# Optimization experiments

Hardware: AMD Instinct MI355X
Metric: run time of the kernel (lower is better)

Reference implementation:

```python
import jax, jax.numpy as jnp
import numpy as np

B, L, D, MAXL = 4, 2048, 1024, 4096

def setup_inputs() -> dict:
    key = jax.random.key(0)
    ks = jax.random.split(key, 7)
    x = jax.random.normal(ks[0], (B, L, D), dtype=jnp.float32)
    mask = jnp.ones((B, 1, L), dtype=jnp.int32)
    # kv_proj: Linear(D,D) -> ReLU -> Linear(D, 2D)
    s1 = 1.0 / np.sqrt(D)
    W1 = jax.random.uniform(ks[1], (D, D), minval=-s1, maxval=s1, dtype=jnp.float32)
    b1 = jax.random.uniform(ks[2], (D,), minval=-s1, maxval=s1, dtype=jnp.float32)
    W2 = jax.random.uniform(ks[3], (D, 2 * D), minval=-s1, maxval=s1, dtype=jnp.float32)
    b2 = jax.random.uniform(ks[4], (2 * D,), minval=-s1, maxval=s1, dtype=jnp.float32)
    D_to_L = jax.random.normal(ks[5], (D, MAXL), dtype=jnp.float32) * 0.01
    return {"x": x, "mask": mask, "W1": W1, "b1": b1, "W2": W2, "b2": b2, "D_to_L": D_to_L}

def reference(x, mask, W1, b1, W2, b2, D_to_L):
    Lcur = x.shape[1]
    h = jax.nn.relu(x @ W1 + b1)          # [B,L,D]
    kv = h @ W2 + b2                       # [B,L,2D]
    k, value = jnp.split(kv, 2, axis=-1)   # [B,L,D] each
    scores = jnp.einsum('bld,dk->blk', k, D_to_L[:, :Lcur])  # [B,L,L]
    scores = jnp.where(mask == 0, -jnp.inf, scores)
    attention = jax.nn.softmax(scores, axis=-1)
    output = attention @ value             # [B,L,D]
    return output, attention
```

## Files before the change

### kernel.cpp

```cpp
#include <hip/hip_runtime.h>
#include <cstdint>
#include <cstddef>

__device__ __forceinline__ float bf2f(uint16_t u) {
    union { uint32_t i; float f; } w; w.i = ((uint32_t)u) << 16; return w.f;
}
__device__ __forceinline__ uint16_t f2bf(float f) {
    union { float f; uint32_t i; } w; w.f = f;
    uint32_t x = w.i;
    uint32_t r = (x + 0x7FFFu + ((x >> 16) & 1u)) >> 16;
    return (uint16_t)r;
}

typedef __bf16 bf16x8 __attribute__((ext_vector_type(8)));
typedef float  f32x4  __attribute__((ext_vector_type(4)));

__device__ __forceinline__ void load_lds16(const void* gptr, void* lptr) {
    __builtin_amdgcn_global_load_lds(
        (__attribute__((address_space(1))) void*)gptr,
        (__attribute__((address_space(3))) void*)lptr,
        16, 0, 0);
}

template<int AFP32, int OUTFP32, int RELU>
__global__ __launch_bounds__(256, 3)
void gemm_bt(const void* __restrict__ Av, const uint16_t* __restrict__ BT,
             const float* __restrict__ bias, void* __restrict__ Cv,
             int K, int lda, int ldb, int ldc,
             long long sA, long long sB, long long sC)
{
    __shared__ uint16_t As[128 * 32];
    __shared__ uint16_t Bs[128 * 32];

    const int nx = (int)gridDim.x, ny = (int)gridDim.y, nz = (int)gridDim.z;
    const int g   = (int)blockIdx.x + nx * ((int)blockIdx.y + ny * (int)blockIdx.z);
    const int xcd = g & 7;
    const int ii  = g >> 3;
    const int xz  = 8 / nz;
    const int bz  = xcd / xz;
    const int sub = xcd % xz;
    const int ypc = ny / xz;
    const int by  = sub * ypc + ii % ypc;
    const int bx  = ii / ypc;

    const int t    = threadIdx.x;
    const int lane = t & 63;
    const int w    = t >> 6;
    const int quad = lane >> 4;
    const int l15  = lane & 15;
    const int wr   = w >> 1;
    const int wc   = w & 1;
    const int gm0  = by * 128;
    const int gn0  = bx * 128;

    BT += (long long)bz * sB;

    f32x4 acc[4][4] = {};

    const int ch_r = lane >> 2;
    const int ch_c = (lane & 3) * 8;

    for (int k0 = 0; k0 < K; k0 += 32) {
        __syncthreads();

        {
            int row = w * 16 + ch_r;
            load_lds16(BT + (size_t)(gn0 + row) * ldb + k0 + ch_c, (void*)(Bs + w * 512));
            load_lds16(BT + (size_t)(gn0 + row + 64) * ldb + k0 + ch_c, (void*)(Bs + (w + 4) * 512));
        }
        if (AFP32) {
            const float* A = (const float*)Av + (long long)bz * sA;
            const int row = t >> 1, half = t & 1;
            const float* ap = A + (size_t)(gm0 + row) * lda + k0 + half * 16;
            float4 f0 = ((const float4*)ap)[0];
            float4 f1 = ((const float4*)ap)[1];
            float4 f2 = ((const float4*)ap)[2];
            float4 f3 = ((const float4*)ap)[3];
            union { __bf16 h[16]; uint4 q[2]; } u;
            u.h[0]  = (__bf16)f0.x; u.h[1]  = (__bf16)f0.y;
            u.h[2]  = (__bf16)f0.z; u.h[3]  = (__bf16)f0.w;
            u.h[4]  = (__bf16)f1.x; u.h[5]  = (__bf16)f1.y;
            u.h[6]  = (__bf16)f1.z; u.h[7]  = (__bf16)f1.w;
            u.h[8]  = (__bf16)f2.x; u.h[9]  = (__bf16)f2.y;
            u.h[10] = (__bf16)f2.z; u.h[11] = (__bf16)f2.w;
            u.h[12] = (__bf16)f3.x; u.h[13] = (__bf16)f3.y;
            u.h[14] = (__bf16)f3.z; u.h[15] = (__bf16)f3.w;
            uint4* d = (uint4*)(As + row * 32 + half * 16);
            d[0] = u.q[0];
            d[1] = u.q[1];
        } else {
            const uint16_t* A = (const uint16_t*)Av + (long long)bz * sA;
            int row = w * 16 + ch_r;
            load_lds16(A + (size_t)(gm0 + row) * lda + k0 + ch_c, (void*)(As + w * 512));
            load_lds16(A + (size_t)(gm0 + row + 64) * lda + k0 + ch_c, (void*)(As + (w + 4) * 512));
        }
        __syncthreads();

        bf16x8 af[4], bfr[4];
#pragma unroll
        for (int i = 0; i < 4; i++) {
            af[i]  = *(const bf16x8*)(As + (wr * 64 + i * 16 + l15) * 32 + quad * 8);
            bfr[i] = *(const bf16x8*)(Bs + (wc * 64 + i * 16 + l15) * 32 + quad * 8);
        }
#pragma unroll
        for (int mi = 0; mi < 4; mi++)
#pragma unroll
            for (int ni = 0; ni < 4; ni++)
                acc[mi][ni] = __builtin_amdgcn_mfma_f32_16x16x32_bf16(af[mi], bfr[ni], acc[mi][ni], 0, 0, 0);
    }

#pragma unroll
    for (int ni = 0; ni < 4; ni++) {
        const int gcol = gn0 + wc * 64 + ni * 16 + l15;
        const float bv = bias ? bias[gcol] : 0.0f;
#pragma unroll
        for (int mi = 0; mi < 4; mi++) {
#pragma unroll
            for (int r = 0; r < 4; r++) {
                const int grow = gm0 + wr * 64 + mi * 16 + quad * 4 + r;
                float v = acc[mi][ni][r] + bv;
                if (RELU) v = fmaxf(v, 0.0f);
                if (OUTFP32) {
                    float* C = (float*)Cv + (long long)bz * sC;
                    C[(size_t)grow * ldc + gcol] = v;
                } else {
                    uint16_t* C = (uint16_t*)Cv + (long long)bz * sC;
                    C[(size_t)grow * ldc + gcol] = f2bf(v);
                }
            }
        }
    }
}

__global__ __launch_bounds__(256)
void transpose_f32_to_bf16(const float* __restrict__ src, uint16_t* __restrict__ dst,
                           int src_ld, int dst_ld)
{
    __shared__ uint16_t tile[64 * 65];
    const int k0 = blockIdx.y * 64, n0 = blockIdx.x * 64;
    const int t = threadIdx.x;
#pragma unroll
    for (int i = 0; i < 16; i++) {
        int idx = i * 256 + t;
        int r = idx >> 6, c = idx & 63;
        tile[c * 65 + r] = f2bf(src[(size_t)(k0 + r) * src_ld + n0 + c]);
    }
    __syncthreads();
#pragma unroll
    for (int i = 0; i < 16; i++) {
        int idx = i * 256 + t;
        int n = idx >> 6, k = idx & 63;
        dst[(size_t)(n0 + n) * dst_ld + k0 + k] = tile[n * 65 + k];
    }
}

__global__ __launch_bounds__(256)
void transpose_bf16(const uint16_t* __restrict__ src, uint16_t* __restrict__ dst,
                    int src_ld, int dst_ld, long long sS, long long sD)
{
    __shared__ uint16_t tile[64 * 65];
    src += (long long)blockIdx.z * sS;
    dst += (long long)blockIdx.z * sD;
    const int k0 = blockIdx.y * 64, n0 = blockIdx.x * 64;
    const int t = threadIdx.x;
#pragma unroll
    for (int i = 0; i < 16; i++) {
        int idx = i * 256 + t;
        int r = idx >> 6, c = idx & 63;
        tile[c * 65 + r] = src[(size_t)(k0 + r) * src_ld + n0 + c];
    }
    __syncthreads();
#pragma unroll
    for (int i = 0; i < 16; i++) {
        int idx = i * 256 + t;
        int n = idx >> 6, k = idx & 63;
        dst[(size_t)(n0 + n) * dst_ld + k0 + k] = tile[n * 65 + k];
    }
}

__global__ __launch_bounds__(256)
void softmax_rows_f32(float* __restrict__ S, uint16_t* __restrict__ Sbf,
                      const int* __restrict__ mask, int L)
{
    const int row = blockIdx.x;
    const int b = row >> 11;
    float* rp = S + (size_t)row * L;
    uint16_t* bp = Sbf + (size_t)row * L;
    const int* mrow = mask + (size_t)b * L;
    const int t = threadIdx.x;
    const int c0 = t * 8;

    float v[8];
    *(float4*)(v + 0) = *(const float4*)(rp + c0);
    *(float4*)(v + 4) = *(const float4*)(rp + c0 + 4);
    bool mk[8];
    float lmax = -1e30f;
#pragma unroll
    for (int j = 0; j < 8; j++) {
        mk[j] = (mrow[c0 + j] != 0);
        if (mk[j]) lmax = fmaxf(lmax, v[j]);
    }
#pragma unroll
    for (int off = 32; off > 0; off >>= 1)
        lmax = fmaxf(lmax, __shfl_xor(lmax, off, 64));

    __shared__ float redm[4];
    __shared__ float reds[4];
    const int w = t >> 6, lane = t & 63;
    if (lane == 0) redm[w] = lmax;
    __syncthreads();
    lmax = fmaxf(fmaxf(redm[0], redm[1]), fmaxf(redm[2], redm[3]));

    float e[8];
    float lsum = 0.f;
#pragma unroll
    for (int j = 0; j < 8; j++) {
        e[j] = mk[j] ? __expf(v[j] - lmax) : 0.0f;
        lsum += e[j];
    }
#pragma unroll
    for (int off = 32; off > 0; off >>= 1)
        lsum += __shfl_xor(lsum, off, 64);
    if (lane == 0) reds[w] = lsum;
    __syncthreads();
    lsum = reds[0] + reds[1] + reds[2] + reds[3];

    const float inv = 1.0f / lsum;
    uint16_t ub[8];
#pragma unroll
    for (int j = 0; j < 8; j++) {
        v[j] = e[j] * inv;
        ub[j] = f2bf(v[j]);
    }
    *(float4*)(rp + c0)     = *(const float4*)(v + 0);
    *(float4*)(rp + c0 + 4) = *(const float4*)(v + 4);
    *(uint4*)(bp + c0)      = *(const uint4*)ub;
}

extern "C" void kernel_launch(void* const* d_in, const int* in_sizes, int n_in,
                              void* d_out, int out_size, void* d_ws, size_t ws_size,
                              hipStream_t stream)
{
    const float* x    = (const float*)d_in[0];
    const int*   mask = (const int*)d_in[1];
    const float* W1   = (const float*)d_in[2];
    const float* b1   = (const float*)d_in[3];
    const float* W2   = (const float*)d_in[4];
    const float* b2   = (const float*)d_in[5];
    const float* D2L  = (const float*)d_in[6];

    const int Lr = 2048, D = 1024, M = 4 * Lr;
    float* outp = (float*)d_out;
    float* attn = outp + (size_t)M * D;

    uint16_t* W1T  = (uint16_t*)d_ws;
    uint16_t* W2T  = W1T + 1024 * 1024;
    uint16_t* D2LT = W2T + 2048 * 1024;
    uint16_t* hbuf = D2LT + 2048 * 1024;
    uint16_t* kv   = hbuf + (size_t)M * D;
    uint16_t* vT   = hbuf;
    uint16_t* abf  = kv;

    dim3 blk(256);

    transpose_f32_to_bf16<<<dim3(16, 16), blk, 0, stream>>>(W1,  W1T,  1024, 1024);
    transpose_f32_to_bf16<<<dim3(32, 16), blk, 0, stream>>>(W2,  W2T,  2048, 1024);
    transpose_f32_to_bf16<<<dim3(32, 16), blk, 0, stream>>>(D2L, D2LT, 4096, 1024);

    gemm_bt<1, 0, 1><<<dim3(8, 64, 1), blk, 0, stream>>>(x, W1T, b1, hbuf,
        1024, 1024, 1024, 1024, 0, 0, 0);

    gemm_bt<0, 0, 0><<<dim3(16, 64, 1), blk, 0, stream>>>(hbuf, W2T, b2, kv,
        1024, 1024, 1024, 2048, 0, 0, 0);

    transpose_bf16<<<dim3(16, 32, 4), blk, 0, stream>>>(kv + 1024, vT,
        2048, 2048, (long long)2048 * 2048, (long long)1024 * 2048);

    gemm_bt<0, 1, 0><<<dim3(16, 64, 1), blk, 0, stream>>>(kv, D2LT, nullptr, attn,
        1024, 2048, 1024, 2048, 0, 0, 0);

    softmax_rows_f32<<<dim3(8192), blk, 0, stream>>>(attn, abf, mask, Lr);

    gemm_bt<0, 1, 0><<<dim3(8, 16, 4), blk, 0, stream>>>(abf, vT, nullptr, outp,
        2048, 2048, 2048, 1024,
        (long long)2048 * 2048, (long long)1024 * 2048, (long long)2048 * 1024);
}
```

Baseline: 359.1 us.

## Fold key projection into D_to_L product and fuse value/score GEMMs

Precomputes W2_k @ D_to_L (plus a column bias b2_k @ D_to_L) so the scores come straight from h in one GEMM that is concatenated with the value projection, removing the separate k materialization and the K=1024 score GEMM. Scores are written as bf16 and softmax reads bf16 plus the bias, which cuts fp32 score traffic. x is cast to bf16 up front instead of being converted inside the GEMM. Extra rounding of the fused weight and of the bf16 scores may lower accuracy.

```diff
diff --git a/kernel.cpp b/kernel.cpp
--- a/kernel.cpp
+++ b/kernel.cpp
@@ -22,12 +22,13 @@
         16, 0, 0);
 }
 
-template<int AFP32, int OUTFP32, int RELU>
+template<int OUTFP32, int RELU, int SPLIT>
 __global__ __launch_bounds__(256, 3)
-void gemm_bt(const void* __restrict__ Av, const uint16_t* __restrict__ BT,
+void gemm_bt(const uint16_t* __restrict__ A, const uint16_t* __restrict__ BT,
              const float* __restrict__ bias, void* __restrict__ Cv,
              int K, int lda, int ldb, int ldc,
-             long long sA, long long sB, long long sC)
+             long long sA, long long sB, long long sC,
+             void* __restrict__ C2v, int ldc2, int ncut)
 {
     __shared__ uint16_t As[128 * 32];
     __shared__ uint16_t Bs[128 * 32];
@@ -53,6 +54,7 @@
     const int gm0  = by * 128;
     const int gn0  = bx * 128;
 
+    A  += (long long)bz * sA;
     BT += (long long)bz * sB;
 
     f32x4 acc[4][4] = {};
@@ -62,35 +64,10 @@
 
     for (int k0 = 0; k0 < K; k0 += 32) {
         __syncthreads();
-
         {
             int row = w * 16 + ch_r;
             load_lds16(BT + (size_t)(gn0 + row) * ldb + k0 + ch_c, (void*)(Bs + w * 512));
             load_lds16(BT + (size_t)(gn0 + row + 64) * ldb + k0 + ch_c, (void*)(Bs + (w + 4) * 512));
-        }
-        if (AFP32) {
-            const float* A = (const float*)Av + (long long)bz * sA;
-            const int row = t >> 1, half = t & 1;
-            const float* ap = A + (size_t)(gm0 + row) * lda + k0 + half * 16;
-            float4 f0 = ((const float4*)ap)[0];
-            float4 f1 = ((const float4*)ap)[1];
-            float4 f2 = ((const float4*)ap)[2];
-            float4 f3 = ((const float4*)ap)[3];
-            union { __bf16 h[16]; uint4 q[2]; } u;
-            u.h[0]  = (__bf16)f0.x; u.h[1]  = (__bf16)f0.y;
-            u.h[2]  = (__bf16)f0.z; u.h[3]  = (__bf16)f0.w;
-            u.h[4]  = (__bf16)f1.x; u.h[5]  = (__bf16)f1.y;
-            u.h[6]  = (__bf16)f1.z; u.h[7]  = (__bf16)f1.w;
-            u.h[8]  = (__bf16)f2.x; u.h[9]  = (__bf16)f2.y;
-            u.h[10] = (__bf16)f2.z; u.h[11] = (__bf16)f2.w;
-            u.h[12] = (__bf16)f3.x; u.h[13] = (__bf16)f3.y;
-            u.h[14] = (__bf16)f3.z; u.h[15] = (__bf16)f3.w;
-            uint4* d = (uint4*)(As + row * 32 + half * 16);
-            d[0] = u.q[0];
-            d[1] = u.q[1];
-        } else {
-            const uint16_t* A = (const uint16_t*)Av + (long long)bz * sA;
-            int row = w * 16 + ch_r;
             load_lds16(A + (size_t)(gm0 + row) * lda + k0 + ch_c, (void*)(As + w * 512));
             load_lds16(A + (size_t)(gm0 + row + 64) * lda + k0 + ch_c, (void*)(As + (w + 4) * 512));
         }
@@ -109,10 +86,11 @@
                 acc[mi][ni] = __builtin_amdgcn_mfma_f32_16x16x32_bf16(af[mi], bfr[ni], acc[mi][ni], 0, 0, 0);
     }
 
+    const bool to2 = SPLIT && (gn0 >= ncut);
 #pragma unroll
     for (int ni = 0; ni < 4; ni++) {
         const int gcol = gn0 + wc * 64 + ni * 16 + l15;
-        const float bv = bias ? bias[gcol] : 0.0f;
+        const float bv = (!to2 && bias) ? bias[gcol] : 0.0f;
 #pragma unroll
         for (int mi = 0; mi < 4; mi++) {
 #pragma unroll
@@ -120,7 +98,10 @@
                 const int grow = gm0 + wr * 64 + mi * 16 + quad * 4 + r;
                 float v = acc[mi][ni][r] + bv;
                 if (RELU) v = fmaxf(v, 0.0f);
-                if (OUTFP32) {
+                if (to2) {
+                    uint16_t* C2 = (uint16_t*)C2v;
+                    C2[(size_t)grow * ldc2 + (gcol - ncut)] = f2bf(v);
+                } else if (OUTFP32) {
                     float* C = (float*)Cv + (long long)bz * sC;
                     C[(size_t)grow * ldc + gcol] = v;
                 } else {
@@ -133,6 +114,33 @@
 }
 
 __global__ __launch_bounds__(256)
+void cast_f32_bf16(const float* __restrict__ src, uint16_t* __restrict__ dst)
+{
+    const size_t i = ((size_t)blockIdx.x * 256 + threadIdx.x) * 8;
+    float4 f0 = *(const float4*)(src + i);
+    float4 f1 = *(const float4*)(src + i + 4);
+    uint16_t u[8];
+    u[0] = f2bf(f0.x); u[1] = f2bf(f0.y); u[2] = f2bf(f0.z); u[3] = f2bf(f0.w);
+    u[4] = f2bf(f1.x); u[5] = f2bf(f1.y); u[6] = f2bf(f1.z); u[7] = f2bf(f1.w);
+    *(uint4*)(dst + i) = *(const uint4*)u;
+}
+
+__global__ __launch_bounds__(256)
+void cast2d_f32_bf16(const float* __restrict__ src, uint16_t* __restrict__ dst,
+                     int src_ld, int C)
+{
+    const size_t i = ((size_t)blockIdx.x * 256 + threadIdx.x) * 8;
+    const int r = (int)(i / C), c = (int)(i % C);
+    const float* sp = src + (size_t)r * src_ld + c;
+    float4 f0 = *(const float4*)sp;
+    float4 f1 = *(const float4*)(sp + 4);
+    uint16_t u[8];
+    u[0] = f2bf(f0.x); u[1] = f2bf(f0.y); u[2] = f2bf(f0.z); u[3] = f2bf(f0.w);
+    u[4] = f2bf(f1.x); u[5] = f2bf(f1.y); u[6] = f2bf(f1.z); u[7] = f2bf(f1.w);
+    *(uint4*)(dst + i) = *(const uint4*)u;
+}
+
+__global__ __launch_bounds__(256)
 void transpose_f32_to_bf16(const float* __restrict__ src, uint16_t* __restrict__ dst,
                            int src_ld, int dst_ld)
 {
@@ -179,25 +187,40 @@
 }
 
 __global__ __launch_bounds__(256)
-void softmax_rows_f32(float* __restrict__ S, uint16_t* __restrict__ Sbf,
-                      const int* __restrict__ mask, int L)
+void colbias(const float* __restrict__ b2, const float* __restrict__ D2L,
+             float* __restrict__ out)
+{
+    const int l = blockIdx.x * 256 + threadIdx.x;
+    float acc = 0.f;
+#pragma unroll 8
+    for (int d = 0; d < 1024; d++)
+        acc = fmaf(b2[d], D2L[(size_t)d * 4096 + l], acc);
+    out[l] = acc;
+}
+
+__global__ __launch_bounds__(256)
+void softmax_rows(const uint16_t* __restrict__ Sin_, float* __restrict__ Aout,
+                  uint16_t* __restrict__ Abf, const float* __restrict__ bs,
+                  const int* __restrict__ mask, int L)
 {
     const int row = blockIdx.x;
     const int b = row >> 11;
-    float* rp = S + (size_t)row * L;
-    uint16_t* bp = Sbf + (size_t)row * L;
+    const uint16_t* sp = Sin_ + (size_t)row * L;
+    float* op = Aout + (size_t)row * L;
+    uint16_t* bp = Abf + (size_t)row * L;
     const int* mrow = mask + (size_t)b * L;
     const int t = threadIdx.x;
     const int c0 = t * 8;
 
+    uint16_t su[8];
+    *(uint4*)su = *(const uint4*)(sp + c0);
     float v[8];
-    *(float4*)(v + 0) = *(const float4*)(rp + c0);
-    *(float4*)(v + 4) = *(const float4*)(rp + c0 + 4);
     bool mk[8];
     float lmax = -1e30f;
 #pragma unroll
     for (int j = 0; j < 8; j++) {
         mk[j] = (mrow[c0 + j] != 0);
+        v[j] = bf2f(su[j]) + bs[c0 + j];
         if (mk[j]) lmax = fmaxf(lmax, v[j]);
     }
 #pragma unroll
@@ -232,8 +255,8 @@
         v[j] = e[j] * inv;
         ub[j] = f2bf(v[j]);
     }
-    *(float4*)(rp + c0)     = *(const float4*)(v + 0);
-    *(float4*)(rp + c0 + 4) = *(const float4*)(v + 4);
+    *(float4*)(op + c0)     = *(const float4*)(v + 0);
+    *(float4*)(op + c0 + 4) = *(const float4*)(v + 4);
     *(uint4*)(bp + c0)      = *(const uint4*)ub;
 }
 
@@ -253,35 +276,42 @@
     float* outp = (float*)d_out;
     float* attn = outp + (size_t)M * D;
 
-    uint16_t* W1T  = (uint16_t*)d_ws;
-    uint16_t* W2T  = W1T + 1024 * 1024;
-    uint16_t* D2LT = W2T + 2048 * 1024;
-    uint16_t* hbuf = D2LT + 2048 * 1024;
-    uint16_t* kv   = hbuf + (size_t)M * D;
-    uint16_t* vT   = hbuf;
-    uint16_t* abf  = kv;
+    uint16_t* W1T    = (uint16_t*)d_ws;
+    uint16_t* BTcat  = W1T   + 1024 * 1024;
+    uint16_t* D2LT   = BTcat + 3072 * 1024;
+    uint16_t* W2kbf  = D2LT  + 2048 * 1024;
+    float*    bias_s = (float*)(W2kbf + 1024 * 1024);
+    uint16_t* xbf    = (uint16_t*)(bias_s + 2048);
+    uint16_t* hbuf   = xbf  + (size_t)M * D;
+    uint16_t* Vbuf   = hbuf + (size_t)M * D;
+    uint16_t* Sbf    = Vbuf + (size_t)M * D;
+    uint16_t* vT     = Sbf  + (size_t)M * 2048;
 
     dim3 blk(256);
 
-    transpose_f32_to_bf16<<<dim3(16, 16), blk, 0, stream>>>(W1,  W1T,  1024, 1024);
-    transpose_f32_to_bf16<<<dim3(32, 16), blk, 0, stream>>>(W2,  W2T,  2048, 1024);
+    cast_f32_bf16<<<dim3(4096), blk, 0, stream>>>(x, xbf);
+    transpose_f32_to_bf16<<<dim3(16, 16), blk, 0, stream>>>(W1, W1T, 1024, 1024);
+    transpose_f32_to_bf16<<<dim3(16, 16), blk, 0, stream>>>(W2 + 1024, BTcat, 2048, 1024);
     transpose_f32_to_bf16<<<dim3(32, 16), blk, 0, stream>>>(D2L, D2LT, 4096, 1024);
-
-    gemm_bt<1, 0, 1><<<dim3(8, 64, 1), blk, 0, stream>>>(x, W1T, b1, hbuf,
-        1024, 1024, 1024, 1024, 0, 0, 0);
-
-    gemm_bt<0, 0, 0><<<dim3(16, 64, 1), blk, 0, stream>>>(hbuf, W2T, b2, kv,
-        1024, 1024, 1024, 2048, 0, 0, 0);
-
-    transpose_bf16<<<dim3(16, 32, 4), blk, 0, stream>>>(kv + 1024, vT,
-        2048, 2048, (long long)2048 * 2048, (long long)1024 * 2048);
-
-    gemm_bt<0, 1, 0><<<dim3(16, 64, 1), blk, 0, stream>>>(kv, D2LT, nullptr, attn,
-        1024, 2048, 1024, 2048, 0, 0, 0);
-
-    softmax_rows_f32<<<dim3(8192), blk, 0, stream>>>(attn, abf, mask, Lr);
-
-    gemm_bt<0, 1, 0><<<dim3(8, 16, 4), blk, 0, stream>>>(abf, vT, nullptr, outp,
+    cast2d_f32_bf16<<<dim3(512), blk, 0, stream>>>(W2, W2kbf, 2048, 1024);
+    colbias<<<dim3(8), blk, 0, stream>>>(b2, D2L, bias_s);
+
+    gemm_bt<0, 0, 0><<<dim3(8, 16, 1), blk, 0, stream>>>(D2LT, W2kbf, nullptr,
+        BTcat + 1024 * 1024, 1024, 1024, 1024, 1024, 0, 0, 0, nullptr, 0, 0);
+
+    gemm_bt<0, 1, 0><<<dim3(8, 64, 1), blk, 0, stream>>>(xbf, W1T, b1, hbuf,
+        1024, 1024, 1024, 1024, 0, 0, 0, nullptr, 0, 0);
+
+    gemm_bt<0, 0, 1><<<dim3(24, 64, 1), blk, 0, stream>>>(hbuf, BTcat, b2 + 1024, Vbuf,
+        1024, 1024, 1024, 1024, 0, 0, 0, Sbf, 2048, 1024);
+
+    transpose_bf16<<<dim3(16, 32, 4), blk, 0, stream>>>(Vbuf, vT,
+        1024, 2048, (long long)2048 * 1024, (long long)1024 * 2048);
+
+    softmax_rows<<<dim3(8192), blk, 0, stream>>>(Sbf, attn, Sbf, bias_s, mask, Lr);
+
+    gemm_bt<1, 0, 0><<<dim3(8, 16, 4), blk, 0, stream>>>(Sbf, vT, nullptr, outp,
         2048, 2048, 2048, 1024,
-        (long long)2048 * 2048, (long long)1024 * 2048, (long long)2048 * 1024);
-}
+        (long long)2048 * 2048, (long long)1024 * 2048, (long long)2048 * 1024,
+        nullptr, 0, 0);
+}
```

Result: slower. 399.8 us (+11.3%).
